# Kernel optimization log

Measured on AMD Instinct MI355X. Metric: run time of the kernel, lower is better.

## Reference

```python
import jax, jax.numpy as jnp
import numpy as np

N_NODES = 50000
N_EDGES = 300000
INPUT_DIM = 128
HIDDEN_DIM = 256
NUM_HEADS = 8
HEAD_DIM = HIDDEN_DIM // NUM_HEADS  # 32
NUM_EDGE_TYPES = 3


def setup_inputs() -> dict:
    key = jax.random.key(0)
    ks = jax.random.split(key, 12)
    s_in = 1.0 / np.sqrt(INPUT_DIM)
    s_hid = 1.0 / np.sqrt(HIDDEN_DIM)
    return {
        "node_features": jax.random.normal(ks[0], (N_NODES, INPUT_DIM), jnp.float32),
        "edges": jax.random.randint(ks[1], (N_EDGES, 2), 0, N_NODES),
        "edge_types": jax.random.randint(ks[2], (N_EDGES,), 0, NUM_EDGE_TYPES),
        # torch.nn.Linear convention: y = x @ W.T + b, W: [out, in]
        "Wq": jax.random.normal(ks[3], (HIDDEN_DIM, INPUT_DIM), jnp.float32) * s_in,
        "bq": jax.random.normal(ks[4], (HIDDEN_DIM,), jnp.float32) * s_in,
        "Wk": jax.random.normal(ks[5], (HIDDEN_DIM, INPUT_DIM), jnp.float32) * s_in,
        "bk": jax.random.normal(ks[6], (HIDDEN_DIM,), jnp.float32) * s_in,
        "Wv": jax.random.normal(ks[7], (HIDDEN_DIM, INPUT_DIM), jnp.float32) * s_in,
        "bv": jax.random.normal(ks[8], (HIDDEN_DIM,), jnp.float32) * s_in,
        "edge_emb": jax.random.normal(ks[9], (NUM_EDGE_TYPES, HIDDEN_DIM), jnp.float32),
        "Wo": jax.random.normal(ks[10], (INPUT_DIM, HIDDEN_DIM), jnp.float32) * s_hid,
        "bo": jax.random.normal(ks[11], (INPUT_DIM,), jnp.float32) * s_hid,
    }


def reference(node_features, edges, edge_types, Wq, bq, Wk, bk, Wv, bv, edge_emb, Wo, bo):
    # Project all nodes once, split heads: [N, H, D]
    Q = (node_features @ Wq.T + bq).reshape(-1, NUM_HEADS, HEAD_DIM)
    K = (node_features @ Wk.T + bk).reshape(-1, NUM_HEADS, HEAD_DIM)
    V = (node_features @ Wv.T + bv).reshape(-1, NUM_HEADS, HEAD_DIM)

    src = edges[:, 0]
    tgt = edges[:, 1]

    # Per-edge small attention: Q[src] [E,H,D] x K[tgt]^T -> [E,H,H]
    # (identical math to the original per-edge-type loop, since only the
    #  edge embedding depends on edge_type and it is gathered per edge)
    scale = 1.0 / jnp.sqrt(jnp.float32(HEAD_DIM))
    scores = jnp.einsum("ehd,egd->ehg", Q[src], K[tgt]) * scale
    attn = jax.nn.softmax(scores, axis=-1)
    msg = jnp.einsum("ehg,egd->ehd", attn, V[tgt]).reshape(-1, HIDDEN_DIM)  # [E, HID]

    msg = msg + edge_emb[edge_types]          # per-edge-type embedding add
    out_e = msg @ Wo.T + bo                   # output projection per edge [E, IN]

    # Scatter-add over source nodes (original Python loop over edges)
    messages = jax.ops.segment_sum(out_e, src, num_segments=N_NODES)
    return messages
```

## Files before the change

### kernel.cpp

```cpp
#include <hip/hip_runtime.h>
#include <hip/hip_bf16.h>

#define N_NODES 50000
#define N_EDGES 300000
#define M_PAD 50048
#define M_PAD2 50176
#define NBLK 196
#define SC 0.17677669529663687f

#define MB_CONV 6250
#define MB_HIST 1172
#define MB_PREP 513

typedef __attribute__((ext_vector_type(8))) short bf16x8;
typedef __attribute__((ext_vector_type(4))) short bf16x4;
typedef __attribute__((ext_vector_type(4))) float f32x4;

__device__ __forceinline__ unsigned short f2bf(float x) {
    unsigned int u = __float_as_uint(x);
    unsigned int r = (u + 0x7FFFu + ((u >> 16) & 1u)) >> 16;
    return (unsigned short)r;
}
__device__ __forceinline__ short bfs(float x) {
    __hip_bfloat16 h = __float2bfloat16(x);
    return *reinterpret_cast<short*>(&h);
}

__global__ __launch_bounds__(512)
void qkv_gemm(const unsigned short* __restrict__ A2, const unsigned short* __restrict__ B2,
              const float* __restrict__ biasCat,
              unsigned short* __restrict__ Qb, unsigned short* __restrict__ Kb,
              unsigned short* __restrict__ Vb)
{
    constexpr int K2 = 128;
    const int t    = threadIdx.x;
    const int w    = t >> 6;
    const int lane = t & 63;
    const int l15  = lane & 15;
    const int lg   = lane >> 4;
    const int bx   = blockIdx.x;
    const int m0   = blockIdx.y * 128;
    const int wm   = (w >> 2) * 64;
    const int wn   = (w & 3) * 64;
    const float mulc = (bx == 0) ? SC : 1.0f;

    f32x4 acc[4][4] = {};

    const unsigned short* Abase = A2 + (size_t)(m0 + wm + l15) * K2 + lg * 8;
    const unsigned short* Bbase = B2 + (size_t)(bx * 256 + wn + l15) * K2 + lg * 8;

    #pragma unroll 2
    for (int ks = 0; ks < K2 / 32; ++ks) {
        bf16x8 af[4], bfv[4];
        #pragma unroll
        for (int mi = 0; mi < 4; ++mi)
            af[mi] = *(const bf16x8*)(Abase + (size_t)mi * 16 * K2 + ks * 32);
        #pragma unroll
        for (int ni = 0; ni < 4; ++ni)
            bfv[ni] = *(const bf16x8*)(Bbase + (size_t)ni * 16 * K2 + ks * 32);
        #pragma unroll
        for (int mi = 0; mi < 4; ++mi)
            #pragma unroll
            for (int ni = 0; ni < 4; ++ni)
                acc[mi][ni] = __builtin_amdgcn_mfma_f32_16x16x32_bf16(
                    af[mi], bfv[ni], acc[mi][ni], 0, 0, 0);
    }

    __shared__ unsigned short Cs[64 * 256];
    float bvn[4];
    #pragma unroll
    for (int ni = 0; ni < 4; ++ni)
        bvn[ni] = biasCat[bx * 256 + wn + ni * 16 + l15];

    #pragma unroll
    for (int p = 0; p < 2; ++p) {
        if (p) __syncthreads();
        #pragma unroll
        for (int mi2 = 0; mi2 < 2; ++mi2) {
            const int mi = p * 2 + mi2;
            #pragma unroll
            for (int j = 0; j < 4; ++j) {
                const int lr = (wm >> 1) + mi2 * 16 + lg * 4 + j;
                const int xr = (lr & 7) << 3;
                #pragma unroll
                for (int ni = 0; ni < 4; ++ni) {
                    const int col = wn + ni * 16 + l15;
                    Cs[lr * 256 + (col ^ xr)] = f2bf(fmaf(acc[mi][ni][j], mulc, bvn[ni]));
                }
            }
        }
        __syncthreads();

        if (bx < 2) {
            unsigned short* dst = bx ? Kb : Qb;
            #pragma unroll
            for (int c8 = 0; c8 < 4; ++c8) {
                const int chunk = c8 * 512 + t;
                const int lr = chunk >> 5;
                const int ec = (chunk & 31) * 8;
                const int gr = m0 + ((lr < 32) ? (p * 32 + lr)
                                               : (64 + p * 32 + (lr - 32)));
                const bf16x8 v = *(const bf16x8*)&Cs[lr * 256 + (ec ^ ((lr & 7) << 3))];
                *(bf16x8*)&dst[(size_t)gr * 256 + ec] = v;
            }
        } else {
            #pragma unroll
            for (int c8 = 0; c8 < 4; ++c8) {
                const int chunk = c8 * 512 + t;
                const int lr = chunk >> 5;
                const int ec = (chunk & 31) * 8;
                const int gr = m0 + ((lr < 32) ? (p * 32 + lr)
                                               : (64 + p * 32 + (lr - 32)));
                const int d  = ec >> 3;
                const int xr = (lr & 7) << 3;
                bf16x8 v;
                #pragma unroll
                for (int g = 0; g < 8; ++g)
                    v[g] = (short)Cs[lr * 256 + ((g * 32 + d) ^ xr)];
                *(bf16x8*)&Vb[(size_t)gr * 256 + ec] = v;
            }
        }
    }
}

__global__ __launch_bounds__(128)
void out_gemm(const unsigned short* __restrict__ accQ, const unsigned short* __restrict__ B2o,
              const float* __restrict__ eew, const float* __restrict__ bo,
              const float4* __restrict__ cnt4, float* __restrict__ Cout)
{
    const int t    = threadIdx.x;
    const int w    = t >> 6;
    const int lane = t & 63;
    const int l15  = lane & 15;
    const int lg   = lane >> 4;
    const int m0   = blockIdx.y * 32;
    const int wn   = w * 64;

    f32x4 acc[2][4] = {};

    const unsigned short* Abase = accQ + (size_t)(m0 + l15) * 256 + lg * 8;
    const unsigned short* Bbase = B2o + (size_t)(wn + l15) * 256 + lg * 8;

    #pragma unroll 2
    for (int ks = 0; ks < 8; ++ks) {
        bf16x8 af[2], bfv[4];
        #pragma unroll
        for (int mi = 0; mi < 2; ++mi)
            af[mi] = *(const bf16x8*)(Abase + (size_t)mi * 16 * 256 + ks * 32);
        #pragma unroll
        for (int ni = 0; ni < 4; ++ni)
            bfv[ni] = *(const bf16x8*)(Bbase + (size_t)ni * 16 * 256 + ks * 32);
        #pragma unroll
        for (int mi = 0; mi < 2; ++mi)
            #pragma unroll
            for (int ni = 0; ni < 4; ++ni)
                acc[mi][ni] = __builtin_amdgcn_mfma_f32_16x16x32_bf16(
                    af[mi], bfv[ni], acc[mi][ni], 0, 0, 0);
    }

    #pragma unroll
    for (int mi = 0; mi < 2; ++mi)
        #pragma unroll
        for (int j = 0; j < 4; ++j) {
            const int row = m0 + mi * 16 + lg * 4 + j;
            if (row < N_NODES) {
                const float4 cv = cnt4[row];
                #pragma unroll
                for (int ni = 0; ni < 4; ++ni) {
                    const int col = wn + ni * 16 + l15;
                    Cout[(size_t)row * 128 + col] = acc[mi][ni][j]
                        + cv.x * eew[col] + cv.y * eew[128 + col]
                        + cv.z * eew[256 + col] + cv.w * bo[col];
                }
            }
        }
}

__global__ __launch_bounds__(256)
void mega_prep(const float4* __restrict__ nf4,
               const int* __restrict__ edges, const int* __restrict__ etypes,
               const float* __restrict__ Wq, const float* __restrict__ Wk,
               const float* __restrict__ Wv, const float* __restrict__ bq,
               const float* __restrict__ bk, const float* __restrict__ bv,
               const float* __restrict__ Wo, const float* __restrict__ ee,
               unsigned short* __restrict__ A2, unsigned short* __restrict__ B2qkv,
               unsigned short* __restrict__ B2o,
               float* __restrict__ biasCat, float* __restrict__ eew,
               int* __restrict__ degType)
{
    const int bid = blockIdx.x, t = threadIdx.x;
    if (bid < MB_CONV) {
        const int tid = bid * 256 + t;
        const int m = tid >> 5, k4 = (tid & 31) * 4;
        const float4 v = nf4[tid];
        ushort4 hi;
        hi.x = f2bf(v.x); hi.y = f2bf(v.y); hi.z = f2bf(v.z); hi.w = f2bf(v.w);
        *reinterpret_cast<ushort4*>(&A2[(size_t)m * 128 + k4]) = hi;
    } else if (bid < MB_CONV + MB_HIST) {
        const int e = (bid - MB_CONV) * 256 + t;
        if (e < N_EDGES) atomicAdd(&degType[edges[2 * e] * 4 + etypes[e]], 1);
    } else {
        const int pbid = bid - MB_CONV - MB_HIST;
        if (pbid < 384) {
            const int tid = pbid * 256 + t;
            const int r = tid >> 7, k = tid & 127;
            const float* W = (r < 256) ? Wq : (r < 512) ? Wk : Wv;
            B2qkv[(size_t)r * 128 + k] = f2bf(W[(size_t)(r & 255) * 128 + k]);
            if (k == 0) {
                const float* b = (r < 256) ? bq : (r < 512) ? bk : bv;
                biasCat[r] = b[r & 255] * ((r < 256) ? SC : 1.0f);
            }
        } else if (pbid < 512) {
            const int tid = (pbid - 384) * 256 + t;
            const int r = tid >> 8, k = tid & 255;
            B2o[(size_t)r * 256 + k] = f2bf(Wo[(size_t)r * 256 + k]);
        } else if (t < 128) {
            float a0 = 0.f, a1 = 0.f, a2 = 0.f;
            for (int k = 0; k < 256; ++k) {
                const float w = Wo[(size_t)t * 256 + k];
                a0 += ee[k] * w; a1 += ee[256 + k] * w; a2 += ee[512 + k] * w;
            }
            eew[t] = a0; eew[128 + t] = a1; eew[256 + t] = a2;
        }
    }
}

__global__ __launch_bounds__(256)
void scan_part1(const int4* __restrict__ degType4, int* __restrict__ blockSum)
{
    const int t = threadIdx.x;
    const int i = blockIdx.x * 256 + t;
    int v = 0;
    if (i < N_NODES) {
        const int4 dt = degType4[i];
        v = dt.x + dt.y + dt.z;
    }
    #pragma unroll
    for (int o = 1; o < 64; o <<= 1) v += __shfl_xor(v, o);
    __shared__ int ws[4];
    if ((t & 63) == 0) ws[t >> 6] = v;
    __syncthreads();
    if (t == 0) blockSum[blockIdx.x] = ws[0] + ws[1] + ws[2] + ws[3];
}

__global__ __launch_bounds__(256)
void scan_part2(const int* __restrict__ blockSum, int* __restrict__ blockBase,
                int* __restrict__ rowStart)
{
    __shared__ int lds[256];
    const int t = threadIdx.x;
    lds[t] = (t < NBLK) ? blockSum[t] : 0;
    __syncthreads();
    #pragma unroll
    for (int o = 1; o < 256; o <<= 1) {
        const int u = (t >= o) ? lds[t - o] : 0;
        __syncthreads();
        lds[t] += u;
        __syncthreads();
    }
    if (t < NBLK) blockBase[t] = (t == 0) ? 0 : lds[t - 1];
    if (t == 0) rowStart[N_NODES] = N_EDGES;
}

__global__ __launch_bounds__(256)
void scan_part3(const int4* __restrict__ degType4, const int* __restrict__ blockBase,
                int* __restrict__ rowStart, int* __restrict__ cursor,
                float4* __restrict__ cnt4)
{
    const int t = threadIdx.x;
    const int lane = t & 63, wid = t >> 6;
    const int i = blockIdx.x * 256 + t;
    int4 dt = make_int4(0, 0, 0, 0);
    if (i < N_NODES) dt = degType4[i];
    const int d = dt.x + dt.y + dt.z;
    int x = d;
    #pragma unroll
    for (int o = 1; o < 64; o <<= 1) {
        const int u = __shfl_up(x, o);
        if (lane >= o) x += u;
    }
    __shared__ int wtot[4];
    if (lane == 63) wtot[wid] = x;
    __syncthreads();
    int wo = 0;
    #pragma unroll
    for (int wi = 0; wi < 3; ++wi) wo += (wi < wid) ? wtot[wi] : 0;
    const int excl = blockBase[blockIdx.x] + wo + x - d;
    if (i < N_NODES) {
        rowStart[i] = excl;
        cursor[i]   = excl;
        cnt4[i]     = make_float4((float)dt.x, (float)dt.y, (float)dt.z, (float)d);
    }
}

__global__ __launch_bounds__(256)
void scatter_kernel(const int* __restrict__ edges, int* __restrict__ cursor,
                    int* __restrict__ packed)
{
    const int e = blockIdx.x * 256 + threadIdx.x;
    if (e < N_EDGES) {
        const int pos = atomicAdd(&cursor[edges[2 * e]], 1);
        packed[pos] = edges[2 * e + 1];
    }
}

__device__ __forceinline__ bf16x4 softmax_pa(f32x4 s, bool valid)
{
    const float e0 = __expf(s[0]), e1 = __expf(s[1]);
    const float e2 = __expf(s[2]), e3 = __expf(s[3]);
    float sum = e0 + e1 + e2 + e3;
    sum += __shfl_xor(sum, 16);
    const float inv = valid ? __builtin_amdgcn_rcpf(sum) : 0.0f;
    bf16x4 pa;
    pa[0] = bfs(e0 * inv);
    pa[1] = bfs(e1 * inv);
    pa[2] = bfs(e2 * inv);
    pa[3] = bfs(e3 * inv);
    return pa;
}

__global__ __launch_bounds__(256)
void node_gather_kernel(const int* __restrict__ packed, const int* __restrict__ rowStart,
                        const unsigned short* __restrict__ Qb,
                        const unsigned short* __restrict__ Kb,
                        const unsigned short* __restrict__ Vb,
                        unsigned short* __restrict__ accQ)
{
    const int lane = threadIdx.x & 63;
    const int n = blockIdx.x * 4 + (threadIdx.x >> 6);
    if (n >= N_NODES) return;
    const int l15 = lane & 15;
    const int lg  = lane >> 4;

    const bf16x8 qf = *(const bf16x8*)&Qb[(size_t)n * 256 + (l15 & 7) * 32 + lg * 8];

    f32x4 cpvA0 = {0.f,0.f,0.f,0.f}, cpvA1 = {0.f,0.f,0.f,0.f};
    f32x4 cpvB0 = {0.f,0.f,0.f,0.f}, cpvB1 = {0.f,0.f,0.f,0.f};

    const int lo = rowStart[n], hi = rowStart[n + 1];
    const bool validBase = ((l15 < 8) == (lg < 2));
    const f32x4 z4 = {0.f, 0.f, 0.f, 0.f};
    int idx = lo;

    for (; idx + 4 <= hi; idx += 4) {
        const int t0 = packed[idx],     t1 = packed[idx + 1];
        const int t2 = packed[idx + 2], t3 = packed[idx + 3];

        const int tkA = (l15 < 8) ? t0 : t1;
        const int tkB = (l15 < 8) ? t2 : t3;
        const bf16x8 kfA = *(const bf16x8*)&Kb[(size_t)tkA * 256 + (l15 & 7) * 32 + lg * 8];
        const bf16x8 kfB = *(const bf16x8*)&Kb[(size_t)tkB * 256 + (l15 & 7) * 32 + lg * 8];

        const int tvA = (lg < 2) ? t0 : t1;
        const int tvB = (lg < 2) ? t2 : t3;
        const unsigned short* vrA = &Vb[(size_t)tvA * 256 + (lg & 1) * 4];
        const unsigned short* vrB = &Vb[(size_t)tvB * 256 + (lg & 1) * 4];
        const bf16x4 vfA0 = *(const bf16x4*)&vrA[l15 * 8];
        const bf16x4 vfA1 = *(const bf16x4*)&vrA[(l15 + 16) * 8];
        const bf16x4 vfB0 = *(const bf16x4*)&vrB[l15 * 8];
        const bf16x4 vfB1 = *(const bf16x4*)&vrB[(l15 + 16) * 8];

        const f32x4 sA = __builtin_amdgcn_mfma_f32_16x16x32_bf16(kfA, qf, z4, 0, 0, 0);
        const f32x4 sB = __builtin_amdgcn_mfma_f32_16x16x32_bf16(kfB, qf, z4, 0, 0, 0);

        const bf16x4 paA = softmax_pa(sA, validBase);
        const bf16x4 paB = softmax_pa(sB, validBase);

        cpvA0 = __builtin_amdgcn_mfma_f32_16x16x16bf16_1k(paA, vfA0, cpvA0, 0, 0, 0);
        cpvA1 = __builtin_amdgcn_mfma_f32_16x16x16bf16_1k(paA, vfA1, cpvA1, 0, 0, 0);
        cpvB0 = __builtin_amdgcn_mfma_f32_16x16x16bf16_1k(paB, vfB0, cpvB0, 0, 0, 0);
        cpvB1 = __builtin_amdgcn_mfma_f32_16x16x16bf16_1k(paB, vfB1, cpvB1, 0, 0, 0);
    }

    for (; idx < hi; idx += 2) {
        const int  t0  = packed[idx];
        const bool dup = (idx + 1 >= hi);
        const int  t1  = dup ? t0 : packed[idx + 1];

        const int tk = (l15 < 8) ? t0 : t1;
        const bf16x8 kf = *(const bf16x8*)&Kb[(size_t)tk * 256 + (l15 & 7) * 32 + lg * 8];

        const int tv = (lg < 2) ? t0 : t1;
        const unsigned short* vrow = &Vb[(size_t)tv * 256 + (lg & 1) * 4];
        const bf16x4 vf0 = *(const bf16x4*)&vrow[l15 * 8];
        const bf16x4 vf1 = *(const bf16x4*)&vrow[(l15 + 16) * 8];

        const f32x4 s = __builtin_amdgcn_mfma_f32_16x16x32_bf16(kf, qf, z4, 0, 0, 0);
        const bool valid = validBase && !(dup && (l15 >= 8));
        const bf16x4 pa = softmax_pa(s, valid);

        cpvA0 = __builtin_amdgcn_mfma_f32_16x16x16bf16_1k(pa, vf0, cpvA0, 0, 0, 0);
        cpvA1 = __builtin_amdgcn_mfma_f32_16x16x16bf16_1k(pa, vf1, cpvA1, 0, 0, 0);
    }

    f32x4 cpv0 = cpvA0 + cpvB0;
    f32x4 cpv1 = cpvA1 + cpvB1;

    #pragma unroll
    for (int j = 0; j < 4; ++j) {
        cpv0[j] += __shfl_xor(cpv0[j], 32);
        cpv1[j] += __shfl_xor(cpv1[j], 32);
    }

    if (lane < 32) {
        unsigned short* row = &accQ[(size_t)n * 256];
        #pragma unroll
        for (int j = 0; j < 4; ++j) {
            const int h = lg * 4 + j;
            row[h * 32 + l15]      = (unsigned short)bfs(cpv0[j]);
            row[h * 32 + 16 + l15] = (unsigned short)bfs(cpv1[j]);
        }
    }
}

extern "C" void kernel_launch(void* const* d_in, const int* in_sizes, int n_in,
                              void* d_out, int out_size, void* d_ws, size_t ws_size,
                              hipStream_t stream)
{
    const float* nf      = (const float*)d_in[0];
    const int*   edges   = (const int*)d_in[1];
    const int*   etypes  = (const int*)d_in[2];
    const float* Wq      = (const float*)d_in[3];
    const float* bq      = (const float*)d_in[4];
    const float* Wk      = (const float*)d_in[5];
    const float* bk      = (const float*)d_in[6];
    const float* Wv      = (const float*)d_in[7];
    const float* bv      = (const float*)d_in[8];
    const float* ee      = (const float*)d_in[9];
    const float* Wo      = (const float*)d_in[10];
    const float* bo      = (const float*)d_in[11];
    float* out = (float*)d_out;

    char* ws = (char*)d_ws;
    size_t off = 0;
    auto alloc = [&](size_t bytes) -> void* {
        void* p = ws + off;
        off = (off + bytes + 255) & ~(size_t)255;
        return p;
    };
    unsigned short* A2     = (unsigned short*)alloc((size_t)M_PAD * 128 * 2);
    unsigned short* B2qkv  = (unsigned short*)alloc((size_t)768 * 128 * 2);
    unsigned short* B2o    = (unsigned short*)alloc((size_t)128 * 256 * 2);
    float*          biasC  = (float*)alloc(768 * sizeof(float));
    float*          eew    = (float*)alloc(384 * sizeof(float));
    unsigned short* Qb     = (unsigned short*)alloc((size_t)M_PAD * 256 * 2);
    unsigned short* Kb     = (unsigned short*)alloc((size_t)M_PAD * 256 * 2);
    unsigned short* Vb     = (unsigned short*)alloc((size_t)M_PAD * 256 * 2);
    unsigned short* accQ   = (unsigned short*)alloc((size_t)M_PAD2 * 256 * 2);
    float4* cnt4    = (float4*)alloc((size_t)N_NODES * sizeof(float4));
    int*    degType = (int*)alloc((size_t)N_NODES * 4 * sizeof(int));
    int*    rowS    = (int*)alloc((size_t)(N_NODES + 1) * sizeof(int));
    int*    curs    = (int*)alloc((size_t)N_NODES * sizeof(int));
    int*    pck     = (int*)alloc((size_t)N_EDGES * sizeof(int));
    int*    bSum    = (int*)alloc((size_t)NBLK * sizeof(int));
    int*    bBase   = (int*)alloc((size_t)NBLK * sizeof(int));

    const dim3 blk(256);

    hipMemsetAsync(degType, 0, (size_t)N_NODES * 4 * sizeof(int), stream);
    mega_prep<<<dim3(MB_CONV + MB_HIST + MB_PREP), blk, 0, stream>>>(
        (const float4*)nf, edges, etypes, Wq, Wk, Wv, bq, bk, bv, Wo, ee,
        A2, B2qkv, B2o, biasC, eew, degType);

    scan_part1<<<dim3(NBLK), blk, 0, stream>>>((const int4*)degType, bSum);
    scan_part2<<<dim3(1), blk, 0, stream>>>(bSum, bBase, rowS);
    scan_part3<<<dim3(NBLK), blk, 0, stream>>>((const int4*)degType, bBase, rowS, curs, cnt4);
    scatter_kernel<<<dim3((N_EDGES + 255) / 256), blk, 0, stream>>>(edges, curs, pck);

    qkv_gemm<<<dim3(3, M_PAD / 128), dim3(512), 0, stream>>>(
        A2, B2qkv, biasC, Qb, Kb, Vb);

    node_gather_kernel<<<dim3((N_NODES + 3) / 4), blk, 0, stream>>>(
        pck, rowS, Qb, Kb, Vb, accQ);

    out_gemm<<<dim3(1, M_PAD2 / 32), dim3(128), 0, stream>>>(
        accQ, B2o, eew, bo, cnt4, out);
}
```

Baseline: 178.5 us.

## Fuse edge scatter into QKV GEMM and stage swizzled A tile via LDS

The separate scatter kernel becomes extra blocks appended to the QKV GEMM launch, which saves one launch and lets the scatter atomics overlap with GEMM work. The GEMM's A operand is now loaded into LDS with global_load_lds direct copies. The prep kernel writes A2 in an XOR-swizzled layout so the LDS fragment reads avoid bank conflicts. LDS is reused for the epilogue staging buffer. This adds a block barrier and a dependency on the swizzled A2 layout.

```diff
diff --git a/kernel.cpp b/kernel.cpp
--- a/kernel.cpp
+++ b/kernel.cpp
@@ -12,9 +12,18 @@
 #define MB_HIST 1172
 #define MB_PREP 513
 
+#define QKV_BLOCKS 1173
+#define SCAT_BLOCKS 586
+
 typedef __attribute__((ext_vector_type(8))) short bf16x8;
 typedef __attribute__((ext_vector_type(4))) short bf16x4;
 typedef __attribute__((ext_vector_type(4))) float f32x4;
+
+typedef __attribute__((address_space(3))) unsigned int lds_uint;
+typedef const __attribute__((address_space(1))) unsigned int glb_uint;
+__device__ __forceinline__ void gld16(const void* g, void* l) {
+    __builtin_amdgcn_global_load_lds((glb_uint*)g, (lds_uint*)l, 16, 0, 0);
+}
 
 __device__ __forceinline__ unsigned short f2bf(float x) {
     unsigned int u = __float_as_uint(x);
@@ -30,34 +39,59 @@
 void qkv_gemm(const unsigned short* __restrict__ A2, const unsigned short* __restrict__ B2,
               const float* __restrict__ biasCat,
               unsigned short* __restrict__ Qb, unsigned short* __restrict__ Kb,
-              unsigned short* __restrict__ Vb)
-{
-    constexpr int K2 = 128;
-    const int t    = threadIdx.x;
+              unsigned short* __restrict__ Vb,
+              const int* __restrict__ edges, int* __restrict__ cursor,
+              int* __restrict__ packed)
+{
+    __shared__ unsigned short SMEM[128 * 128];
+    const int bid = blockIdx.x;
+    const int t   = threadIdx.x;
+
+    if (bid >= QKV_BLOCKS) {
+        const int e = (bid - QKV_BLOCKS) * 512 + t;
+        if (e < N_EDGES) {
+            const int pos = atomicAdd(&cursor[edges[2 * e]], 1);
+            packed[pos] = edges[2 * e + 1];
+        }
+        return;
+    }
+
     const int w    = t >> 6;
     const int lane = t & 63;
     const int l15  = lane & 15;
     const int lg   = lane >> 4;
-    const int bx   = blockIdx.x;
-    const int m0   = blockIdx.y * 128;
+    const int bx   = bid % 3;
+    const int m0   = (bid / 3) * 128;
     const int wm   = (w >> 2) * 64;
     const int wn   = (w & 3) * 64;
     const float mulc = (bx == 0) ? SC : 1.0f;
 
+    {
+        const char* srcbase = (const char*)A2 + (size_t)m0 * 256;
+        #pragma unroll
+        for (int i = 0; i < 4; ++i) {
+            const int cb = (i * 8 + w) * 1024;
+            gld16(srcbase + cb + lane * 16, (char*)SMEM + cb);
+        }
+    }
+
     f32x4 acc[4][4] = {};
-
-    const unsigned short* Abase = A2 + (size_t)(m0 + wm + l15) * K2 + lg * 8;
-    const unsigned short* Bbase = B2 + (size_t)(bx * 256 + wn + l15) * K2 + lg * 8;
-
-    #pragma unroll 2
-    for (int ks = 0; ks < K2 / 32; ++ks) {
+    const unsigned short* Bbase = B2 + (size_t)(bx * 256 + wn + l15) * 128 + lg * 8;
+
+    __syncthreads();
+
+    #pragma unroll
+    for (int ks = 0; ks < 4; ++ks) {
         bf16x8 af[4], bfv[4];
         #pragma unroll
-        for (int mi = 0; mi < 4; ++mi)
-            af[mi] = *(const bf16x8*)(Abase + (size_t)mi * 16 * K2 + ks * 32);
-        #pragma unroll
         for (int ni = 0; ni < 4; ++ni)
-            bfv[ni] = *(const bf16x8*)(Bbase + (size_t)ni * 16 * K2 + ks * 32);
+            bfv[ni] = *(const bf16x8*)(Bbase + (size_t)ni * 16 * 128 + ks * 32);
+        #pragma unroll
+        for (int mi = 0; mi < 4; ++mi) {
+            const int r    = wm + mi * 16 + l15;
+            const int slot = (ks * 4 + lg) ^ ((r & 7) << 1);
+            af[mi] = *(const bf16x8*)((const char*)SMEM + r * 256 + slot * 16);
+        }
         #pragma unroll
         for (int mi = 0; mi < 4; ++mi)
             #pragma unroll
@@ -66,7 +100,9 @@
                     af[mi], bfv[ni], acc[mi][ni], 0, 0, 0);
     }
 
-    __shared__ unsigned short Cs[64 * 256];
+    __syncthreads();
+
+    unsigned short* Cs = SMEM;
     float bvn[4];
     #pragma unroll
     for (int ni = 0; ni < 4; ++ni)
@@ -195,7 +231,10 @@
         const float4 v = nf4[tid];
         ushort4 hi;
         hi.x = f2bf(v.x); hi.y = f2bf(v.y); hi.z = f2bf(v.z); hi.w = f2bf(v.w);
-        *reinterpret_cast<ushort4*>(&A2[(size_t)m * 128 + k4]) = hi;
+        const int chunk = k4 >> 3;
+        const int sub   = k4 & 7;
+        const int scol  = ((chunk ^ ((m & 7) << 1)) << 3) + sub;
+        *reinterpret_cast<ushort4*>(&A2[(size_t)m * 128 + scol]) = hi;
     } else if (bid < MB_CONV + MB_HIST) {
         const int e = (bid - MB_CONV) * 256 + t;
         if (e < N_EDGES) atomicAdd(&degType[edges[2 * e] * 4 + etypes[e]], 1);
@@ -293,17 +332,6 @@
     }
 }
 
-__global__ __launch_bounds__(256)
-void scatter_kernel(const int* __restrict__ edges, int* __restrict__ cursor,
-                    int* __restrict__ packed)
-{
-    const int e = blockIdx.x * 256 + threadIdx.x;
-    if (e < N_EDGES) {
-        const int pos = atomicAdd(&cursor[edges[2 * e]], 1);
-        packed[pos] = edges[2 * e + 1];
-    }
-}
-
 __device__ __forceinline__ bf16x4 softmax_pa(f32x4 s, bool valid)
 {
     const float e0 = __expf(s[0]), e1 = __expf(s[1]);
@@ -465,10 +493,9 @@
     scan_part1<<<dim3(NBLK), blk, 0, stream>>>((const int4*)degType, bSum);
     scan_part2<<<dim3(1), blk, 0, stream>>>(bSum, bBase, rowS);
     scan_part3<<<dim3(NBLK), blk, 0, stream>>>((const int4*)degType, bBase, rowS, curs, cnt4);
-    scatter_kernel<<<dim3((N_EDGES + 255) / 256), blk, 0, stream>>>(edges, curs, pck);
-
-    qkv_gemm<<<dim3(3, M_PAD / 128), dim3(512), 0, stream>>>(
-        A2, B2qkv, biasC, Qb, Kb, Vb);
+
+    qkv_gemm<<<dim3(QKV_BLOCKS + SCAT_BLOCKS), dim3(512), 0, stream>>>(
+        A2, B2qkv, biasC, Qb, Kb, Vb, edges, curs, pck);
 
     node_gather_kernel<<<dim3((N_NODES + 3) / 4), blk, 0, stream>>>(
         pck, rowS, Qb, Kb, Vb, accQ);
```

Measured after the change: 161.6 us. 1.1x faster.
